# Kernel optimization log

Measured on AMD Instinct MI355X. Metric: run time of the kernel, lower is better.

Reference implementation:

```python
import jax, jax.numpy as jnp
import numpy as np

B, N, K, DIMS, F_DIMS = 2, 32768, 16, 2, 32
DS, DH, DO = 32, 32, 32
DA = DS + DH                      # 64
CH = (DIMS + 1) * (1 + K) + DIMS  # 53
CONV_IN = DIMS + (1 + K) * DA     # 1090
CONV_OUT = (1 + K) * DO           # 544


def setup_inputs() -> dict:
    key = jax.random.key(0)
    ks = jax.random.split(key, 6)
    s = 0.05
    return {
        "pc": jax.random.normal(ks[0], (B, N, 1 + K, DIMS), jnp.float32),
        "feats": jax.random.normal(ks[1], (B, N, 1 + K, F_DIMS), jnp.float32),
        "W_mlp": jax.random.normal(ks[2], (CH, DS), jnp.float32) * s,
        "b_mlp": jnp.zeros((DS,), jnp.float32),
        "W_att": jax.random.normal(ks[3], (DA, DA), jnp.float32) * s,
        "b_att": jnp.zeros((DA,), jnp.float32),
        "W_conv": jax.random.normal(ks[4], (CONV_IN, CONV_OUT), jnp.float32) * s,
        "b_conv": jnp.zeros((CONV_OUT,), jnp.float32),
        "W_skip": jax.random.normal(ks[5], (DO + F_DIMS, DO), jnp.float32) * s,
        "b_skip": jnp.zeros((DO,), jnp.float32),
    }


def reference(pc, feats, W_mlp, b_mlp, W_att, b_att, W_conv, b_conv, W_skip, b_skip):
    # ---- LocSE: relative-position encoding ----
    # rpbn_i[b,n,j] = concat(pc[b,n,i] - pc[b,n,j], ||pc[b,n,j]||)
    norms = jnp.linalg.norm(pc, axis=-1, keepdims=True)          # (B,N,1+K,1)
    # diffs[b,n,j,i,:] = pc[b,n,i,:] - pc[b,n,j,:]
    diffs = pc[:, :, None, :, :] - pc[:, :, :, None, :]          # (B,N,1+K,1+K,dims)
    norms_b = jnp.broadcast_to(norms[:, :, :, None, :], diffs.shape[:-1] + (1,))
    blocks = jnp.concatenate([diffs, norms_b], axis=-1)          # (B,N,1+K,1+K,dims+1)
    blocks = blocks.reshape(pc.shape[:3] + ((1 + K) * (DIMS + 1),))
    rppe = jnp.concatenate([pc, blocks], axis=-1)                # (B,N,1+K,CH)
    r = jax.nn.relu(rppe @ W_mlp + b_mlp)                        # (B,N,1+K,DS)
    se = jnp.concatenate([r, feats], axis=-1)                    # (B,N,1+K,DA)

    # ---- attention pooling (softmax over channel axis) ----
    att = jax.nn.softmax(se @ W_att + b_att, axis=-1) * se       # (B,N,1+K,DA)
    reshaped = att.reshape(att.shape[0], att.shape[1], (1 + K) * DA)

    cat = jnp.concatenate([pc[:, :, 0], reshaped], axis=-1)      # (B,N,CONV_IN)
    res = jax.nn.relu(cat @ W_conv + b_conv)                     # (B,N,(1+K)*DO)
    res = res.reshape(res.shape[0], res.shape[1], 1 + K, DO)

    skip_in = jnp.concatenate([feats, res], axis=-1)             # (B,N,1+K,F+DO)
    skip = jax.nn.relu(skip_in @ W_skip + b_skip)                # (B,N,1+K,DO)
    return skip
```

## Files before the change

kernel.cpp:

```cpp
#include <hip/hip_runtime.h>
#include <hip/hip_bf16.h>
#include <cstdint>

#define KNB      17
#define CH       53
#define MP       16
#define BM       64
#define NTHR     512
#define NRT      17
#define SE_LD    72
#define CATW     1120
#define RES_LD   552
#define NCHUNK   18

#define NE_CONV  (35*34*512)
#define NE_MLP   (2*2*512)
#define NE_ATT   (2*4*512)
#define NE_SKIP  (2*2*512)
#define WS_MLP   (NE_CONV)
#define WS_ATT   (WS_MLP + NE_MLP)
#define WS_SKIP  (WS_ATT + NE_ATT)
#define WS_TOTAL (WS_SKIP + NE_SKIP)

typedef __bf16 bf16x8 __attribute__((ext_vector_type(8)));
typedef float  f32x4  __attribute__((ext_vector_type(4)));
typedef unsigned short u16x4 __attribute__((ext_vector_type(4)));
typedef unsigned short u16x8 __attribute__((ext_vector_type(8)));

__device__ __forceinline__ unsigned short f2b(float f) {
    union { __bf16 h; unsigned short u; } v; v.h = (__bf16)f; return v.u;
}
__device__ __forceinline__ float b2f(unsigned short b) {
    union { unsigned u; float f; } v; v.u = ((unsigned)b) << 16;
    return v.f;
}
__device__ __forceinline__ void gload_lds16(const void* g, void* l) {
    __builtin_amdgcn_global_load_lds(
        (const __attribute__((address_space(1))) unsigned int*)g,
        (__attribute__((address_space(3))) unsigned int*)l, 16, 0, 0);
}

__global__ void seac_prep(const float* __restrict__ Wmlp, const float* __restrict__ Watt,
                          const float* __restrict__ Wconv, const float* __restrict__ Wskip,
                          unsigned short* __restrict__ ws)
{
    int i = blockIdx.x * 256 + threadIdx.x;
    if (i >= WS_TOTAL) return;
    float v;
    if (i < WS_MLP) {
        int idx = i;
        int jj = idx & 7, l = (idx >> 3) & 63, t = idx >> 9;
        int nt = t % 34, ks = t / 34;
        int k = 32*ks + 8*(l >> 4) + jj;
        int o = 16*nt + (l & 15);
        int ok;
        if (k < 1088)       ok = k + 2;
        else if (k == 1088) ok = 0;
        else if (k == 1089) ok = 1;
        else                ok = -1;
        v = (ok >= 0) ? Wconv[ok*544 + o] : 0.f;
    } else if (i < WS_ATT) {
        int idx = i - WS_MLP;
        int jj = idx & 7, l = (idx >> 3) & 63, t = idx >> 9;
        int nt = t & 1, ks = t >> 1;
        int k = 32*ks + 8*(l >> 4) + jj;
        int o = 16*nt + (l & 15);
        v = (k < CH) ? Wmlp[k*32 + o] : 0.f;
    } else if (i < WS_SKIP) {
        int idx = i - WS_ATT;
        int jj = idx & 7, l = (idx >> 3) & 63, t = idx >> 9;
        int nt = t & 3, ks = t >> 2;
        int k = 32*ks + 8*(l >> 4) + jj;
        int o = 16*nt + (l & 15);
        v = Watt[k*64 + o];
    } else {
        int idx = i - WS_SKIP;
        int jj = idx & 7, l = (idx >> 3) & 63, t = idx >> 9;
        int nt = t & 1, ks = t >> 1;
        int k = 32*ks + 8*(l >> 4) + jj;
        int o = 16*nt + (l & 15);
        v = Wskip[k*32 + o];
    }
    ws[i] = f2b(v);
}

__global__ __launch_bounds__(NTHR, 6) void seac_locse(
    const float* __restrict__ pc, const float* __restrict__ feats,
    const float* __restrict__ bmlp, const float* __restrict__ batt,
    const unsigned short* __restrict__ ws, unsigned short* __restrict__ catg,
    int pt0)
{
    __shared__ unsigned short se_l[272 * SE_LD];
    __shared__ float pcl[MP][KNB][2];
    __shared__ float bmlp_l[32];
    __shared__ float batt_l[64];

    const int tid  = threadIdx.x;
    const int w    = tid >> 6;
    const int l    = tid & 63;
    const int g    = l >> 4;
    const int c15  = l & 15;
    const long pbase = (long)pt0 + (long)blockIdx.x * MP;
    const bf16x8* wsB8 = (const bf16x8*)ws;

    if (tid < MP*KNB) {
        int p = tid / KNB, i = tid - p*KNB;
        float x = pc[(pbase + p)*(KNB*2) + 2*i];
        float y = pc[(pbase + p)*(KNB*2) + 2*i + 1];
        pcl[p][i][0] = x; pcl[p][i][1] = y;
    }
    for (int q = tid; q < MP*544/4; q += NTHR) {
        float4 f = *(const float4*)&feats[pbase*544 + 4*q];
        int e0 = 4*q; int p = e0 / 544; int rem = e0 - 544*p;
        int j = rem >> 5, c = rem & 31;
        u16x4 u; u[0] = f2b(f.x); u[1] = f2b(f.y); u[2] = f2b(f.z); u[3] = f2b(f.w);
        *(u16x4*)&se_l[(p*KNB + j)*SE_LD + 32 + c] = u;
    }
    if (tid < 32)                     bmlp_l[tid]      = bmlp[tid];
    else if (tid >= 64 && tid < 128)  batt_l[tid-64]   = batt[tid-64];
    __syncthreads();

    {
        bf16x8 Bm[2][2];
        #pragma unroll
        for (int ks = 0; ks < 2; ++ks)
            #pragma unroll
            for (int nt = 0; nt < 2; ++nt)
                Bm[ks][nt] = wsB8[(WS_MLP >> 3) + (ks*2 + nt)*64 + l];
        float bch[2][4];
        #pragma unroll
        for (int nt = 0; nt < 2; ++nt)
            #pragma unroll
            for (int r = 0; r < 4; ++r) bch[nt][r] = bmlp_l[16*nt + 4*g + r];

        for (int mt = w; mt < NRT; mt += 8) {
            int row = 16*mt + c15;
            int p = row / KNB, j = row - p*KNB;
            float pjx = pcl[p][j][0], pjy = pcl[p][j][1];
            float nj = sqrtf(pjx*pjx + pjy*pjy);
            f32x4 acc0 = {0.f,0.f,0.f,0.f}, acc1 = {0.f,0.f,0.f,0.f};
            #pragma unroll
            for (int ks = 0; ks < 2; ++ks) {
                union { unsigned short u[8]; bf16x8 v; } a;
                #pragma unroll
                for (int jj = 0; jj < 8; ++jj) {
                    int k = 32*ks + 8*g + jj;
                    float vv;
                    if (k == 0) vv = pjx;
                    else if (k == 1) vv = pjy;
                    else if (k < CH) {
                        int kk = k - 2, ii = kk/3, t3 = kk - 3*ii;
                        vv = (t3 == 0) ? (pcl[p][ii][0] - pjx)
                           : (t3 == 1) ? (pcl[p][ii][1] - pjy) : nj;
                    } else vv = 0.f;
                    a.u[jj] = f2b(vv);
                }
                acc0 = __builtin_amdgcn_mfma_f32_16x16x32_bf16(Bm[ks][0], a.v, acc0, 0, 0, 0);
                acc1 = __builtin_amdgcn_mfma_f32_16x16x32_bf16(Bm[ks][1], a.v, acc1, 0, 0, 0);
            }
            u16x4 o0, o1;
            #pragma unroll
            for (int r = 0; r < 4; ++r) {
                o0[r] = f2b(fmaxf(acc0[r] + bch[0][r], 0.f));
                o1[r] = f2b(fmaxf(acc1[r] + bch[1][r], 0.f));
            }
            *(u16x4*)&se_l[row*SE_LD + 4*g]      = o0;
            *(u16x4*)&se_l[row*SE_LD + 16 + 4*g] = o1;
        }
    }
    __syncthreads();

    {
        bf16x8 Ba[2][4];
        #pragma unroll
        for (int ks = 0; ks < 2; ++ks)
            #pragma unroll
            for (int nt = 0; nt < 4; ++nt)
                Ba[ks][nt] = wsB8[(WS_ATT >> 3) + (ks*4 + nt)*64 + l];
        float bch[16];
        #pragma unroll
        for (int nt = 0; nt < 4; ++nt)
            #pragma unroll
            for (int r = 0; r < 4; ++r) bch[4*nt+r] = batt_l[16*nt + 4*g + r];

        for (int mt = w; mt < NRT; mt += 8) {
            int row = 16*mt + c15;
            bf16x8 b0 = *(const bf16x8*)&se_l[row*SE_LD + 8*g];
            bf16x8 b1 = *(const bf16x8*)&se_l[row*SE_LD + 32 + 8*g];
            f32x4 acc[4];
            #pragma unroll
            for (int nt = 0; nt < 4; ++nt) {
                f32x4 z = {0.f,0.f,0.f,0.f};
                acc[nt] = __builtin_amdgcn_mfma_f32_16x16x32_bf16(Ba[0][nt], b0, z,       0, 0, 0);
                acc[nt] = __builtin_amdgcn_mfma_f32_16x16x32_bf16(Ba[1][nt], b1, acc[nt], 0, 0, 0);
            }
            float vv[16];
            #pragma unroll
            for (int nt = 0; nt < 4; ++nt)
                #pragma unroll
                for (int r = 0; r < 4; ++r) vv[4*nt+r] = acc[nt][r] + bch[4*nt+r];
            float m = vv[0];
            #pragma unroll
            for (int i = 1; i < 16; ++i) m = fmaxf(m, vv[i]);
            m = fmaxf(m, __shfl_xor(m, 16)); m = fmaxf(m, __shfl_xor(m, 32));
            float s = 0.f;
            #pragma unroll
            for (int i = 0; i < 16; ++i) { vv[i] = __expf(vv[i] - m); s += vv[i]; }
            s += __shfl_xor(s, 16); s += __shfl_xor(s, 32);
            float inv = 1.f / s;
            #pragma unroll
            for (int nt = 0; nt < 4; ++nt) {
                u16x4 sv = *(const u16x4*)&se_l[row*SE_LD + 16*nt + 4*g];
                u16x4 ov;
                #pragma unroll
                for (int r = 0; r < 4; ++r) ov[r] = f2b(vv[4*nt+r]*inv * b2f(sv[r]));
                *(u16x4*)&se_l[row*SE_LD + 16*nt + 4*g] = ov;
            }
        }
    }
    __syncthreads();

    for (int c = tid; c < MP*140; c += NTHR) {
        int p = c / 140, rem = c - 140*p;
        int e = 8*rem;
        u16x8 v;
        if (e < 1088) {
            int row = p*KNB + (e >> 6), col = e & 63;
            v = *(const u16x8*)&se_l[row*SE_LD + col];
        } else {
            #pragma unroll
            for (int q = 0; q < 8; ++q) v[q] = 0;
            if (e == 1088) { v[0] = f2b(pcl[p][0][0]); v[1] = f2b(pcl[p][0][1]); }
        }
        *(u16x8*)&catg[(pbase + p)*CATW + e] = v;
    }
}

__global__ __launch_bounds__(NTHR, 4) void seac_conv(
    const unsigned short* __restrict__ catg, const float* __restrict__ feats,
    const float* __restrict__ bconv, const float* __restrict__ bskip,
    const unsigned short* __restrict__ ws, float* __restrict__ out, int pt0)
{
    __shared__ unsigned short astage[2][2][BM][32];
    __shared__ unsigned short res_l[32 * RES_LD];
    __shared__ float bconv_l[544];

    const int tid  = threadIdx.x;
    const int w    = tid >> 6;
    const int l    = tid & 63;
    const int g    = l >> 4;
    const int c15  = l & 15;
    const long pbase = (long)pt0 + (long)blockIdx.x * BM;
    const bf16x8* wsB8 = (const bf16x8*)ws;

    for (int i = tid; i < 544; i += NTHR) bconv_l[i] = bconv[i];

    const int s_ksl = tid >> 8, s_p = (tid >> 2) & 63, s_gr = tid & 3;
    unsigned short* s_dst0 = &astage[0][0][0][0] + (size_t)(tid & ~63) * 8;
    unsigned short* s_dst1 = &astage[1][0][0][0] + (size_t)(tid & ~63) * 8;
    #define STAGE(c, b)                                                           \
        do {                                                                      \
            int ks_ = 2*(c) + s_ksl;                                              \
            if (ks_ < 35)                                                         \
                gload_lds16(&catg[(pbase + s_p)*CATW + 32*ks_ + 8*s_gr],          \
                            (b) ? s_dst1 : s_dst0);                               \
        } while (0)

    STAGE(0, 0);
    __syncthreads();

    f32x4 acc[4][5];
    #pragma unroll
    for (int mt = 0; mt < 4; ++mt)
        #pragma unroll
        for (int t = 0; t < 5; ++t) { f32x4 z = {0.f,0.f,0.f,0.f}; acc[mt][t] = z; }

    int buf = 0;
    for (int c = 0; c < NCHUNK; ++c) {
        if (c + 1 < NCHUNK) STAGE(c+1, buf^1);
        #pragma unroll
        for (int ksl = 0; ksl < 2; ++ksl) {
            int ks = 2*c + ksl;
            if (ks < 35) {
                bf16x8 a[4];
                #pragma unroll
                for (int mt = 0; mt < 4; ++mt)
                    a[mt] = *(const bf16x8*)&astage[buf][ksl][16*mt + c15][8*g];
                #pragma unroll
                for (int t = 0; t < 5; ++t) {
                    int nt = w + 8*t;
                    if (nt < 34) {
                        bf16x8 b = wsB8[(ks*34 + nt)*64 + l];
                        #pragma unroll
                        for (int mt = 0; mt < 4; ++mt)
                            acc[mt][t] = __builtin_amdgcn_mfma_f32_16x16x32_bf16(a[mt], b, acc[mt][t], 0, 0, 0);
                    }
                }
            }
        }
        __syncthreads();
        buf ^= 1;
    }
    #undef STAGE

    bf16x8 Bs[2][2];
    #pragma unroll
    for (int ks = 0; ks < 2; ++ks)
        #pragma unroll
        for (int nt = 0; nt < 2; ++nt)
            Bs[ks][nt] = wsB8[(WS_SKIP >> 3) + (ks*2 + nt)*64 + l];
    float bs0 = bskip[c15], bs1 = bskip[16 + c15];

    #pragma unroll
    for (int half = 0; half < 2; ++half) {
        #pragma unroll
        for (int t = 0; t < 5; ++t) {
            int nt = w + 8*t;
            if (nt < 34) {
                float bc = bconv_l[16*nt + c15];
                #pragma unroll
                for (int mh = 0; mh < 2; ++mh) {
                    int mt = 2*half + mh;
                    #pragma unroll
                    for (int r = 0; r < 4; ++r)
                        res_l[(16*mh + 4*g + r)*RES_LD + 16*nt + c15] =
                            f2b(fmaxf(acc[mt][t][r] + bc, 0.f));
                }
            }
        }
        __syncthreads();

        const long gofs = pbase*KNB + 544*half;
        for (int tt = 0; tt < 5; ++tt) {
            int mt2 = w + 8*tt;
            if (mt2 < 34) {
                int rr = 16*mt2 + c15;
                int pp = rr / 17, jn = rr - 17*pp;
                float4 f0 = *(const float4*)&feats[(gofs + rr)*32 + 8*g];
                float4 f1 = *(const float4*)&feats[(gofs + rr)*32 + 8*g + 4];
                union { unsigned short u[8]; bf16x8 v; } af;
                af.u[0]=f2b(f0.x); af.u[1]=f2b(f0.y); af.u[2]=f2b(f0.z); af.u[3]=f2b(f0.w);
                af.u[4]=f2b(f1.x); af.u[5]=f2b(f1.y); af.u[6]=f2b(f1.z); af.u[7]=f2b(f1.w);
                bf16x8 ar = *(const bf16x8*)&res_l[pp*RES_LD + 32*jn + 8*g];
                f32x4 z = {0.f,0.f,0.f,0.f};
                f32x4 a0 = __builtin_amdgcn_mfma_f32_16x16x32_bf16(af.v, Bs[0][0], z, 0, 0, 0);
                a0       = __builtin_amdgcn_mfma_f32_16x16x32_bf16(ar,   Bs[1][0], a0, 0, 0, 0);
                f32x4 a1 = __builtin_amdgcn_mfma_f32_16x16x32_bf16(af.v, Bs[0][1], z, 0, 0, 0);
                a1       = __builtin_amdgcn_mfma_f32_16x16x32_bf16(ar,   Bs[1][1], a1, 0, 0, 0);
                #pragma unroll
                for (int r = 0; r < 4; ++r) {
                    long orow = gofs + 16*mt2 + 4*g + r;
                    out[orow*32 + c15]      = fmaxf(a0[r] + bs0, 0.f);
                    out[orow*32 + 16 + c15] = fmaxf(a1[r] + bs1, 0.f);
                }
            }
        }
        if (half == 0) __syncthreads();
    }
}

extern "C" void kernel_launch(void* const* d_in, const int* in_sizes, int n_in,
                              void* d_out, int out_size, void* d_ws, size_t ws_size,
                              hipStream_t stream)
{
    const float* pc    = (const float*)d_in[0];
    const float* feats = (const float*)d_in[1];
    const float* Wmlp  = (const float*)d_in[2];
    const float* bmlp  = (const float*)d_in[3];
    const float* Watt  = (const float*)d_in[4];
    const float* batt  = (const float*)d_in[5];
    const float* Wconv = (const float*)d_in[6];
    const float* bconv = (const float*)d_in[7];
    const float* Wskip = (const float*)d_in[8];
    const float* bskip = (const float*)d_in[9];
    float* out = (float*)d_out;
    unsigned short* ws16 = (unsigned short*)d_ws;

    int npts = in_sizes[0] / (KNB*2);

    size_t frag_bytes = (size_t)WS_TOTAL * 2;
    size_t cat_off    = (frag_bytes + 255) & ~(size_t)255;
    unsigned short* catg = (unsigned short*)((char*)d_ws + cat_off);
    size_t avail = (ws_size > cat_off) ? (ws_size - cat_off) : 0;
    long maxpts = (long)(avail / (CATW * 2));
    long chunk  = (maxpts / BM) * BM;
    if (chunk > npts) chunk = npts;
    if (chunk < BM)   chunk = BM;

    int prep_blocks = (WS_TOTAL + 255) / 256;
    hipLaunchKernelGGL(seac_prep, dim3(prep_blocks), dim3(256), 0, stream,
                       Wmlp, Watt, Wconv, Wskip, ws16);

    for (long base = 0; base < npts; base += chunk) {
        long c = npts - base; if (c > chunk) c = chunk;
        hipLaunchKernelGGL(seac_locse, dim3((int)(c / MP)), dim3(NTHR), 0, stream,
                           pc, feats, bmlp, batt, ws16, catg, (int)base);
        hipLaunchKernelGGL(seac_conv, dim3((int)(c / BM)), dim3(NTHR), 0, stream,
                           catg, feats, bconv, bskip, ws16, out, (int)base);
    }
}
```

Baseline: 335.9 us.

## Replace direct global-to-LDS staging with register-prefetched, padded LDS double buffer

The A-tile staging in the conv GEMM no longer uses global_load_lds into an unpadded buffer. Each thread now prefetches its 16-byte chunk into registers two chunks ahead, writes it into a padded LDS tile (row stride 36), and synchronises with a raw s_barrier after an LDS waitcnt. The padding is meant to cut bank conflicts on the MFMA operand reads, and the deeper prefetch is meant to hide global latency. In exchange it uses more VGPRs and routes the copy through registers, and the hand-written barrier relies on the LDS waitcnt alone to order the writes.

```diff
diff --git a/kernel.cpp b/kernel.cpp
--- a/kernel.cpp
+++ b/kernel.cpp
@@ -12,6 +12,7 @@
 #define CATW     1120
 #define RES_LD   552
 #define NCHUNK   18
+#define AST_LD   36
 
 #define NE_CONV  (35*34*512)
 #define NE_MLP   (2*2*512)
@@ -33,11 +34,6 @@
 __device__ __forceinline__ float b2f(unsigned short b) {
     union { unsigned u; float f; } v; v.u = ((unsigned)b) << 16;
     return v.f;
-}
-__device__ __forceinline__ void gload_lds16(const void* g, void* l) {
-    __builtin_amdgcn_global_load_lds(
-        (const __attribute__((address_space(1))) unsigned int*)g,
-        (__attribute__((address_space(3))) unsigned int*)l, 16, 0, 0);
 }
 
 __global__ void seac_prep(const float* __restrict__ Wmlp, const float* __restrict__ Watt,
@@ -241,7 +237,7 @@
     const float* __restrict__ bconv, const float* __restrict__ bskip,
     const unsigned short* __restrict__ ws, float* __restrict__ out, int pt0)
 {
-    __shared__ unsigned short astage[2][2][BM][32];
+    __shared__ unsigned short astage[2][2][BM][AST_LD];
     __shared__ unsigned short res_l[32 * RES_LD];
     __shared__ float bconv_l[544];
 
@@ -256,17 +252,13 @@
     for (int i = tid; i < 544; i += NTHR) bconv_l[i] = bconv[i];
 
     const int s_ksl = tid >> 8, s_p = (tid >> 2) & 63, s_gr = tid & 3;
-    unsigned short* s_dst0 = &astage[0][0][0][0] + (size_t)(tid & ~63) * 8;
-    unsigned short* s_dst1 = &astage[1][0][0][0] + (size_t)(tid & ~63) * 8;
-    #define STAGE(c, b)                                                           \
-        do {                                                                      \
-            int ks_ = 2*(c) + s_ksl;                                              \
-            if (ks_ < 35)                                                         \
-                gload_lds16(&catg[(pbase + s_p)*CATW + 32*ks_ + 8*s_gr],          \
-                            (b) ? s_dst1 : s_dst0);                               \
-        } while (0)
-
-    STAGE(0, 0);
+    const unsigned short* s_src = &catg[(pbase + s_p)*CATW + 8*s_gr];
+
+    {
+        u16x8 r0 = *(const u16x8*)(s_src + 32*(0 + s_ksl));
+        *(u16x8*)&astage[0][s_ksl][s_p][8*s_gr] = r0;
+    }
+    u16x8 rcur = *(const u16x8*)(s_src + 32*(2 + s_ksl));
     __syncthreads();
 
     f32x4 acc[4][5];
@@ -275,9 +267,16 @@
         #pragma unroll
         for (int t = 0; t < 5; ++t) { f32x4 z = {0.f,0.f,0.f,0.f}; acc[mt][t] = z; }
 
-    int buf = 0;
+    #pragma unroll 2
     for (int c = 0; c < NCHUNK; ++c) {
-        if (c + 1 < NCHUNK) STAGE(c+1, buf^1);
+        u16x8 rnext;
+        if (c + 2 < NCHUNK) {
+            int ksx = 2*(c+2) + s_ksl; if (ksx > 34) ksx = 0;
+            rnext = *(const u16x8*)(s_src + 32*ksx);
+        }
+        if (c + 1 < NCHUNK)
+            *(u16x8*)&astage[(c+1)&1][s_ksl][s_p][8*s_gr] = rcur;
+
         #pragma unroll
         for (int ksl = 0; ksl < 2; ++ksl) {
             int ks = 2*c + ksl;
@@ -285,7 +284,7 @@
                 bf16x8 a[4];
                 #pragma unroll
                 for (int mt = 0; mt < 4; ++mt)
-                    a[mt] = *(const bf16x8*)&astage[buf][ksl][16*mt + c15][8*g];
+                    a[mt] = *(const bf16x8*)&astage[c&1][ksl][16*mt + c15][8*g];
                 #pragma unroll
                 for (int t = 0; t < 5; ++t) {
                     int nt = w + 8*t;
@@ -298,10 +297,13 @@
                 }
             }
         }
-        __syncthreads();
-        buf ^= 1;
-    }
-    #undef STAGE
+        rcur = rnext;
+        asm volatile("s_waitcnt lgkmcnt(0)" ::: "memory");
+        __builtin_amdgcn_s_barrier();
+        __builtin_amdgcn_sched_barrier(0);
+    }
+
+    __syncthreads();
 
     bf16x8 Bs[2][2];
     #pragma unroll
```

Result: slower. 502.8 us (+49.7%).
